# Kernel optimization log

Hardware: AMD Instinct MI355X
Metric: run time of the kernel (lower is better)

The kernel has to match this reference:

```python
import jax, jax.numpy as jnp
import numpy as np

OUT, IN = 4096, 4096
GROUP = 128
N_GROUPS = IN // GROUP  # 32, remainder_cols == 0
BITS_PRIMARY = 4
BITS_RESIDUAL = 2
EPS = 1e-12


def setup_inputs() -> dict:
    key = jax.random.key(0)
    ks = jax.random.split(key, 6)
    return {
        "x": jax.random.normal(ks[0], (4, 2048, IN), dtype=jnp.float32),
        "norms_primary": jax.random.uniform(ks[1], (OUT, N_GROUPS), dtype=jnp.float32),
        "norms_residual": jax.random.uniform(ks[2], (OUT, N_GROUPS), dtype=jnp.float32),
        "bias": jax.random.normal(ks[3], (OUT,), dtype=jnp.float32),
        "idx_primary": jax.random.randint(ks[4], (OUT, N_GROUPS, GROUP), 0, 2 ** BITS_PRIMARY, dtype=jnp.int32),
        "idx_residual": jax.random.randint(ks[5], (OUT, N_GROUPS, GROUP), 0, 2 ** BITS_RESIDUAL, dtype=jnp.int32),
    }


def _dequant(idx, norms, bits):
    # Codebook: symmetric uniform levels in [-1, 1]; TurboQuant stores a
    # unit-direction per group (codes) plus its L2 norm (fp32 scale).
    levels = jnp.linspace(-1.0, 1.0, 2 ** bits, dtype=norms.dtype)
    q = levels[idx]                                             # [O, G, gs]
    unit = q * jax.lax.rsqrt(jnp.sum(q * q, axis=-1, keepdims=True) + EPS)
    w = norms[..., None] * unit                                 # [O, G, gs]
    return w.reshape(w.shape[0], -1)                            # [O, IN]


def reference(x, norms_primary, norms_residual, bias, idx_primary, idx_residual):
    # primary reconstruction + residual correction, then dense matmul
    w = _dequant(idx_primary, norms_primary, BITS_PRIMARY) \
        + _dequant(idx_residual, norms_residual, BITS_RESIDUAL)  # [OUT, IN]
    w = w.astype(x.dtype)
    # F.linear: y = x @ W^T + b
    return jnp.einsum('bsi,oi->bso', x, w) + bias.astype(x.dtype)
```

## Files before the change

kernel.cpp:

```cpp
#include <hip/hip_runtime.h>
#include <hip/hip_bf16.h>
#include <stdint.h>

#define OUT_DIM 4096
#define IN_DIM  4096
#define GROUPSZ 128
#define NGROUPS 32
#define M_TOTAL 8192
#define EPS_Q   1e-12f

#define BM 256
#define BN 256
#define BK 64
#define NT (IN_DIM / BK)

typedef float f32x4   __attribute__((ext_vector_type(4)));
typedef float float4v __attribute__((ext_vector_type(4)));
typedef short bf16x8  __attribute__((ext_vector_type(8)));

static __device__ __forceinline__ short f2bf(float f) {
    union { float f; unsigned u; } v; v.f = f;
    unsigned r = v.u + 0x7fffu + ((v.u >> 16) & 1u);
    return (short)(r >> 16);
}

#define GLOAD16(gp, lp) __builtin_amdgcn_global_load_lds( \
    (const __attribute__((address_space(1))) void*)(gp),  \
    (__attribute__((address_space(3))) void*)(lp), 16, 0, 0)

__global__ __launch_bounds__(256) void dequant_kernel(
    const float* __restrict__ norms_p, const float* __restrict__ norms_r,
    const int* __restrict__ idx_p, const int* __restrict__ idx_r,
    short* __restrict__ W)
{
    const int gid  = (int)((blockIdx.x * 256u + threadIdx.x) >> 6);
    const int lane = threadIdx.x & 63;
    const size_t base = (size_t)gid * GROUPSZ;

    const int ip0 = idx_p[base + lane];
    const int ip1 = idx_p[base + lane + 64];
    const int ir0 = idx_r[base + lane];
    const int ir1 = idx_r[base + lane + 64];

    const float qp0 = -1.f + (2.f / 15.f) * (float)ip0;
    const float qp1 = -1.f + (2.f / 15.f) * (float)ip1;
    const float qr0 = -1.f + (2.f / 3.f)  * (float)ir0;
    const float qr1 = -1.f + (2.f / 3.f)  * (float)ir1;

    float ssp = qp0 * qp0 + qp1 * qp1;
    float ssr = qr0 * qr0 + qr1 * qr1;
    #pragma unroll
    for (int m = 32; m >= 1; m >>= 1) {
        ssp += __shfl_xor(ssp, m);
        ssr += __shfl_xor(ssr, m);
    }
    const float sp = norms_p[gid] / sqrtf(ssp + EPS_Q);
    const float sr = norms_r[gid] / sqrtf(ssr + EPS_Q);

    W[base + lane]      = f2bf(qp0 * sp + qr0 * sr);
    W[base + lane + 64] = f2bf(qp1 * sp + qr1 * sr);
}

__global__ __launch_bounds__(256) void cast_kernel(
    const float* __restrict__ x, short* __restrict__ xb)
{
    const size_t i = ((size_t)blockIdx.x * 256u + threadIdx.x) * 8u;
    float4v a = *(const float4v*)(x + i);
    float4v b = *(const float4v*)(x + i + 4);
    bf16x8 o;
    o[0] = f2bf(a[0]); o[1] = f2bf(a[1]); o[2] = f2bf(a[2]); o[3] = f2bf(a[3]);
    o[4] = f2bf(b[0]); o[5] = f2bf(b[1]); o[6] = f2bf(b[2]); o[7] = f2bf(b[3]);
    *(bf16x8*)(xb + i) = o;
}

template<int HA, int HB>
__device__ __forceinline__ void mfma_quad(f32x4 (&acc)[2][2][4][2],
                                          const bf16x8 (&af)[4][2],
                                          const bf16x8 (&bf)[2][2]) {
#pragma unroll
    for (int m = 0; m < 4; ++m)
#pragma unroll
        for (int n = 0; n < 2; ++n)
#pragma unroll
            for (int kh = 0; kh < 2; ++kh)
                acc[HA][HB][m][n] = __builtin_amdgcn_mfma_f32_16x16x32_bf16(
                    af[m][kh], bf[n][kh], acc[HA][HB][m][n], 0, 0, 0);
}

static __device__ __forceinline__ void rd8(const short* base, int ck0, int ck1,
                                           bf16x8 (&f)[4][2]) {
#pragma unroll
    for (int m = 0; m < 4; ++m) {
        f[m][0] = *(const bf16x8*)(base + m * 1024 + ck0);
        f[m][1] = *(const bf16x8*)(base + m * 1024 + ck1);
    }
}

static __device__ __forceinline__ void rd4(const short* base, int ck0, int ck1,
                                           bf16x8 (&f)[2][2]) {
#pragma unroll
    for (int n = 0; n < 2; ++n) {
        f[n][0] = *(const bf16x8*)(base + n * 1024 + ck0);
        f[n][1] = *(const bf16x8*)(base + n * 1024 + ck1);
    }
}

#define BARRIER()  asm volatile("s_barrier" ::: "memory")
#define LGKM0()    do { asm volatile("s_waitcnt lgkmcnt(0)" ::: "memory"); \
                        __builtin_amdgcn_sched_barrier(0); } while (0)
#define WAITV(N)   asm volatile("s_waitcnt vmcnt(" #N ")" ::: "memory")

__global__ __launch_bounds__(512, 2) void gemm_kernel(
    const short* __restrict__ Ag,
    const short* __restrict__ Bg,
    const float* __restrict__ bias,
    float* __restrict__ C)
{
    __shared__ short lds[65536];

    const int tid  = threadIdx.x;
    const int lane = tid & 63;
    const int wid  = tid >> 6;
    const int wr   = wid >> 2;
    const int wc   = wid & 3;
    const int fr   = lane & 15;
    const int lq   = lane >> 4;

    const int nwg = gridDim.x;
    const int cpx = nwg >> 3;
    const int wg  = ((int)blockIdx.x & 7) * cpx + ((int)blockIdx.x >> 3);
    const int ntile = wg & 15;
    const int mtile = wg >> 4;
    const uint32_t brow = (uint32_t)mtile * BM;
    const uint32_t bcol = (uint32_t)ntile * BN;

    const uint32_t sr_ = (uint32_t)(tid >> 3);
    const uint32_t gc_ = (uint32_t)((tid & 7) ^ ((tid >> 3) & 7));
    const uint32_t aOffB = (brow + sr_) * IN_DIM + gc_ * 8;
    const uint32_t bOffB = (bcol + sr_) * IN_DIM + gc_ * 8;

    auto stage = [&](const short* M, uint32_t baseOff, uint32_t extra, short* dstRegion) {
        GLOAD16(M + baseOff + extra,            dstRegion + tid * 8);
        GLOAD16(M + baseOff + extra + 262144u,  dstRegion + tid * 8 + 4096);
    };

    const int c0  = (lq ^ (fr & 7));
    const int ck0 = c0 * 8;
    const int ck1 = (c0 ^ 4) * 8;
    const int aRd = (wr * 64 + fr) * 64;
    const int bRd = (wc * 32 + fr) * 64;

    f32x4  acc[2][2][4][2] = {};
    bf16x8 af[4][2], bf0[2][2], bf1[2][2];

    stage(Ag, aOffB, 0u,            lds);
    stage(Bg, bOffB, 0u,            lds + 16384);
    stage(Ag, aOffB, 524288u,       lds + 8192);
    stage(Bg, bOffB, 524288u,       lds + 24576);
    stage(Ag, aOffB, 64u,           lds + 32768);
    stage(Bg, bOffB, 64u,           lds + 32768 + 16384);
    WAITV(8);
    BARRIER();

#define TILE_BODY(T, STG0, STG1, STG2, STG3, WAIT_P0, WAIT_P3) do {           \
    short* sb = lds + (((T) & 1) ? 32768 : 0);                                \
    short* ob = lds + (((T) & 1) ? 0 : 32768);                                \
                                                   \
    rd8(sb + aRd, ck0, ck1, af);                                              \
    rd4(sb + 16384 + bRd, ck0, ck1, bf0);                                     \
    if (STG0) stage(Ag, aOffB, 524288u + (uint32_t)((T) + 1) * 64u, ob + 8192); \
    BARRIER(); LGKM0();                                                       \
    __builtin_amdgcn_s_setprio(1); mfma_quad<0,0>(acc, af, bf0);              \
    __builtin_amdgcn_s_setprio(0);                                            \
    WAIT_P0;                                                                  \
    BARRIER();                                                                \
                                                   \
    rd4(sb + 24576 + bRd, ck0, ck1, bf1);                                     \
    if (STG1) stage(Bg, bOffB, 524288u + (uint32_t)((T) + 1) * 64u, ob + 24576); \
    BARRIER(); LGKM0();                                                       \
    __builtin_amdgcn_s_setprio(1); mfma_quad<0,1>(acc, af, bf1);              \
    __builtin_amdgcn_s_setprio(0);                                            \
    BARRIER();                                                                \
                                                   \
    rd8(sb + 8192 + aRd, ck0, ck1, af);                                       \
    if (STG2) stage(Ag, aOffB, (uint32_t)((T) + 2) * 64u, sb);                \
    BARRIER(); LGKM0();                                                       \
    __builtin_amdgcn_s_setprio(1); mfma_quad<1,0>(acc, af, bf0);              \
    __builtin_amdgcn_s_setprio(0);                                            \
    BARRIER();                                                                \
                                                   \
    if (STG3) stage(Bg, bOffB, (uint32_t)((T) + 2) * 64u, sb + 16384);        \
    BARRIER(); LGKM0();                                                       \
    __builtin_amdgcn_s_setprio(1); mfma_quad<1,1>(acc, af, bf1);              \
    __builtin_amdgcn_s_setprio(0);                                            \
    WAIT_P3;                                                                  \
    BARRIER();                                                                \
} while (0)

    #pragma unroll 1
    for (int t = 0; t < NT - 2; ++t) {
        TILE_BODY(t, 1, 1, 1, 1, WAITV(6), WAITV(8));
    }
    TILE_BODY(NT - 2, 1, 1, 0, 0, WAITV(6), WAITV(4));
    TILE_BODY(NT - 1, 0, 0, 0, 0, WAITV(0), (void)0);

    #pragma unroll
    for (int hA = 0; hA < 2; ++hA)
    #pragma unroll
    for (int hB = 0; hB < 2; ++hB)
    #pragma unroll
    for (int n = 0; n < 2; ++n) {
        const int col = (int)bcol + hB * 128 + wc * 32 + n * 16 + fr;
        const float bv = bias[col];
        #pragma unroll
        for (int m = 0; m < 4; ++m) {
            const size_t row0 = (size_t)brow + hA * 128 + wr * 64 + m * 16 + lq * 4;
            #pragma unroll
            for (int r = 0; r < 4; ++r)
                C[(row0 + r) * OUT_DIM + col] = acc[hA][hB][m][n][r] + bv;
        }
    }
#undef TILE_BODY
}

extern "C" void kernel_launch(void* const* d_in, const int* in_sizes, int n_in,
                              void* d_out, int out_size, void* d_ws, size_t ws_size,
                              hipStream_t stream)
{
    const float* x        = (const float*)d_in[0];
    const float* norms_p  = (const float*)d_in[1];
    const float* norms_r  = (const float*)d_in[2];
    const float* bias     = (const float*)d_in[3];
    const int*   idx_p    = (const int*)d_in[4];
    const int*   idx_r    = (const int*)d_in[5];
    float*       out      = (float*)d_out;

    short* xb = (short*)d_ws;
    short* wq = (short*)d_ws + (size_t)M_TOTAL * IN_DIM;

    dequant_kernel<<<(OUT_DIM * NGROUPS) / 4, 256, 0, stream>>>(
        norms_p, norms_r, idx_p, idx_r, wq);

    cast_kernel<<<(int)(((size_t)M_TOTAL * IN_DIM) / (256 * 8)), 256, 0, stream>>>(x, xb);

    gemm_kernel<<<(M_TOTAL / BM) * (OUT_DIM / BN), 512, 0, stream>>>(xb, wq, bias, out);
}
```

Before: 292.8 us.

## Cut per-tile barriers and prefetch second A fragment into separate registers

Removes most of the s_barrier calls inside each K-tile, cutting from about eight per tile to two. It loads the second A-half fragment into a new register array af2 early, with a partial lgkmcnt wait, so its LDS reads overlap the second MFMA quad. The goal is less workgroup synchronization stall and better overlap of LDS reads with MFMA. The cost is extra VGPRs, which at 512 threads and 2 blocks per CU could cause spills or lower occupancy. Fewer barriers also raise the risk of LDS write-after-read races where async stages overwrite buffers other waves may still be reading, such as the STG2 write into sb.

```diff
diff --git a/kernel.cpp b/kernel.cpp
--- a/kernel.cpp
+++ b/kernel.cpp
@@ -106,8 +106,9 @@
 }
 
 #define BARRIER()  asm volatile("s_barrier" ::: "memory")
-#define LGKM0()    do { asm volatile("s_waitcnt lgkmcnt(0)" ::: "memory"); \
-                        __builtin_amdgcn_sched_barrier(0); } while (0)
+#define SCHEDBAR() __builtin_amdgcn_sched_barrier(0)
+#define LGKMC(N)   do { asm volatile("s_waitcnt lgkmcnt(" #N ")" ::: "memory"); \
+                        SCHEDBAR(); } while (0)
 #define WAITV(N)   asm volatile("s_waitcnt vmcnt(" #N ")" ::: "memory")
 
 __global__ __launch_bounds__(512, 2) void gemm_kernel(
@@ -151,7 +152,7 @@
     const int bRd = (wc * 32 + fr) * 64;
 
     f32x4  acc[2][2][4][2] = {};
-    bf16x8 af[4][2], bf0[2][2], bf1[2][2];
+    bf16x8 af[4][2], af2[4][2], bf0[2][2], bf1[2][2];
 
     stage(Ag, aOffB, 0u,            lds);
     stage(Bg, bOffB, 0u,            lds + 16384);
@@ -162,47 +163,43 @@
     WAITV(8);
     BARRIER();
 
-#define TILE_BODY(T, STG0, STG1, STG2, STG3, WAIT_P0, WAIT_P3) do {           \
+#define TILE_BODY(T, STG0, STG1, STG2, STG3, WAIT_MID, WAIT_END, BAR_END) do { \
     short* sb = lds + (((T) & 1) ? 32768 : 0);                                \
     short* ob = lds + (((T) & 1) ? 0 : 32768);                                \
-                                                   \
+                              \
     rd8(sb + aRd, ck0, ck1, af);                                              \
     rd4(sb + 16384 + bRd, ck0, ck1, bf0);                                     \
     if (STG0) stage(Ag, aOffB, 524288u + (uint32_t)((T) + 1) * 64u, ob + 8192); \
-    BARRIER(); LGKM0();                                                       \
+    LGKMC(0);                                                                 \
     __builtin_amdgcn_s_setprio(1); mfma_quad<0,0>(acc, af, bf0);              \
     __builtin_amdgcn_s_setprio(0);                                            \
-    WAIT_P0;                                                                  \
+    WAIT_MID;                                                                 \
     BARRIER();                                                                \
-                                                   \
+                             \
     rd4(sb + 24576 + bRd, ck0, ck1, bf1);                                     \
+    SCHEDBAR();                                                               \
+    rd8(sb + 8192 + aRd, ck0, ck1, af2);                                      \
     if (STG1) stage(Bg, bOffB, 524288u + (uint32_t)((T) + 1) * 64u, ob + 24576); \
-    BARRIER(); LGKM0();                                                       \
+    LGKMC(8);                     \
     __builtin_amdgcn_s_setprio(1); mfma_quad<0,1>(acc, af, bf1);              \
     __builtin_amdgcn_s_setprio(0);                                            \
-    BARRIER();                                                                \
-                                                   \
-    rd8(sb + 8192 + aRd, ck0, ck1, af);                                       \
     if (STG2) stage(Ag, aOffB, (uint32_t)((T) + 2) * 64u, sb);                \
-    BARRIER(); LGKM0();                                                       \
-    __builtin_amdgcn_s_setprio(1); mfma_quad<1,0>(acc, af, bf0);              \
-    __builtin_amdgcn_s_setprio(0);                                            \
-    BARRIER();                                                                \
-                                                   \
+    LGKMC(0);                    \
+    __builtin_amdgcn_s_setprio(1); mfma_quad<1,0>(acc, af2, bf0);             \
+    __builtin_amdgcn_s_setprio(0);                                            \
     if (STG3) stage(Bg, bOffB, (uint32_t)((T) + 2) * 64u, sb + 16384);        \
-    BARRIER(); LGKM0();                                                       \
-    __builtin_amdgcn_s_setprio(1); mfma_quad<1,1>(acc, af, bf1);              \
-    __builtin_amdgcn_s_setprio(0);                                            \
-    WAIT_P3;                                                                  \
-    BARRIER();                                                                \
+    __builtin_amdgcn_s_setprio(1); mfma_quad<1,1>(acc, af2, bf1);             \
+    __builtin_amdgcn_s_setprio(0);                                            \
+    WAIT_END;                                                                 \
+    if (BAR_END) BARRIER();                                                   \
 } while (0)
 
     #pragma unroll 1
     for (int t = 0; t < NT - 2; ++t) {
-        TILE_BODY(t, 1, 1, 1, 1, WAITV(6), WAITV(8));
-    }
-    TILE_BODY(NT - 2, 1, 1, 0, 0, WAITV(6), WAITV(4));
-    TILE_BODY(NT - 1, 0, 0, 0, 0, WAITV(0), (void)0);
+        TILE_BODY(t, 1, 1, 1, 1, WAITV(6), WAITV(8), 1);
+    }
+    TILE_BODY(NT - 2, 1, 1, 0, 0, WAITV(6), WAITV(4), 1);
+    TILE_BODY(NT - 1, 0, 0, 0, 0, WAITV(0), (void)0, 0);
 
     #pragma unroll
     for (int hA = 0; hA < 2; ++hA)
```

Result: faster. 281.2 us (-3.9%).
